# Optimization experiments

Measured on AMD Instinct MI355X. Metric: run time of the kernel, lower is better.

The kernel has to match this reference:

```python
import jax, jax.numpy as jnp
import numpy as np

B, C, H, W, E = 32, 64, 64, 64, 8

def setup_inputs() -> dict:
    key = jax.random.key(0)
    k1, k2, k3 = jax.random.split(key, 3)
    x = jax.random.normal(k1, (B, C, H, W), dtype=jnp.float32)
    gate_w = jax.random.normal(k2, (E, C, 3, 3), dtype=jnp.float32) * 0.02
    gate_b = jnp.zeros((E,), dtype=jnp.float32)
    expert_w = jax.random.normal(k3, (E, C, C), dtype=jnp.float32) * 0.05  # per-expert 1x1 conv (out,in)
    return {"x": x, "gate_w": gate_w, "gate_b": gate_b, "expert_w": expert_w}

def reference(x, gate_w, gate_b, expert_w):
    # Gating: Conv2d(C->E, k=3, stride=1, VALID), then sum over both spatial dims -> [B, E]
    g = jax.lax.conv_general_dilated(
        x, gate_w, window_strides=(1, 1), padding='VALID',
        dimension_numbers=('NCHW', 'OIHW', 'NCHW'))
    g = g + gate_b[None, :, None, None]
    gating_code = jnp.sum(g, axis=(2, 3))                      # [B, E]
    # softmax over experts then top-1
    probs = jax.nn.softmax(gating_code, axis=1)                # [B, E]
    top1_val = jnp.max(probs, axis=1)                          # [B]
    top1_idx = jnp.argmax(probs, axis=1)                       # [B]
    onehot = jax.nn.one_hot(top1_idx, E, dtype=x.dtype)        # [B, E]
    expert_weights = top1_val[:, None] * onehot                # combine tensor squeezed, [B, E]
    dispatch = onehot                                          # bool(combine) cast back to float == one-hot
    # einsum 'bjkd,ben->ebjkd' with n=1: broadcast x to every expert slot, masked by dispatch
    expert_inputs = x[None] * dispatch.T[:, :, None, None, None]   # [E, B, C, H, W]
    # experts: per-expert bias-free 1x1 conv (C -> C)
    expert_out = jnp.einsum('ebchw,efc->ebfhw', expert_inputs, expert_w)  # [E, B, C, H, W]
    # combine: einsum 'ij, ji... -> i...'
    output = jnp.einsum('be,ebchw->bchw', expert_weights, expert_out)      # [B, C, H, W]
    return output, expert_weights
```

## Files before the change

kernel.cpp:

```cpp
#include <hip/hip_runtime.h>

typedef float f4 __attribute__((ext_vector_type(4)));

#define BB 32
#define CC 64
#define EE 8
#define HWX 4096

__global__ __launch_bounds__(256) void k_gate_sums(
    const float* __restrict__ x, const float* __restrict__ gate_w,
    float* __restrict__ gating) {
  __shared__ float sg[9];
  __shared__ float cor[4][4];
  __shared__ float sS[9];
  int t = threadIdx.x;
  int bc = blockIdx.x;
  int c = bc & 63;
  const float* plane = x + (size_t)bc * HWX;
  int h = t >> 2, q = t & 3;
  const f4* rp = (const f4*)(plane + h * 64 + q * 16);
  f4 a0 = rp[0], a1 = rp[1], a2 = rp[2], a3 = rp[3];
  float local = (a0[0]+a0[1]+a0[2]+a0[3]) + (a1[0]+a1[1]+a1[2]+a1[3])
              + (a2[0]+a2[1]+a2[2]+a2[3]) + (a3[0]+a3[1]+a3[2]+a3[3]);
  if (t < 9) sg[t] = 0.f;
  __syncthreads();

  bool special = (h < 2) || (h >= 62);
  int ridx = (h < 2) ? h : h - 60;

  float red = local;
  #pragma unroll
  for (int off = 32; off > 0; off >>= 1) red += __shfl_down(red, off, 64);
  if ((t & 63) == 0) atomicAdd(&sg[0], red);

  if (special) atomicAdd(&sg[1 + ridx], local);
  if (q == 0) {
    atomicAdd(&sg[5], a0[0]); atomicAdd(&sg[6], a0[1]);
    if (special) { cor[ridx][0] = a0[0]; cor[ridx][1] = a0[1]; }
  }
  if (q == 3) {
    atomicAdd(&sg[7], a3[2]); atomicAdd(&sg[8], a3[3]);
    if (special) { cor[ridx][2] = a3[2]; cor[ridx][3] = a3[3]; }
  }
  __syncthreads();

  if (t == 0) {
    const int EX[3][2] = {{2,3},{0,3},{0,1}};
    float T = sg[0];
    #pragma unroll
    for (int i = 0; i < 3; i++)
      #pragma unroll
      for (int j = 0; j < 3; j++) {
        float Re = sg[1 + EX[i][0]] + sg[1 + EX[i][1]];
        float Ce = sg[5 + EX[j][0]] + sg[5 + EX[j][1]];
        float Xc = cor[EX[i][0]][EX[j][0]] + cor[EX[i][0]][EX[j][1]]
                 + cor[EX[i][1]][EX[j][0]] + cor[EX[i][1]][EX[j][1]];
        sS[i * 3 + j] = T - Re - Ce + Xc;
      }
  }
  __syncthreads();

  if (t < EE) {
    const float* gw = gate_w + ((size_t)t * CC + c) * 9;
    float ge = 0.f;
    #pragma unroll
    for (int k = 0; k < 9; k++) ge += gw[k] * sS[k];
    int b = bc >> 6;
    atomicAdd(&gating[b * EE + t], ge);
  }
}

__global__ void k_softmax_top1(const float* __restrict__ gating,
                               const float* __restrict__ gate_b,
                               float* __restrict__ ew_out,
                               float* __restrict__ scale,
                               int* __restrict__ idxb) {
  int b = threadIdx.x;
  if (b >= BB) return;
  float g[EE];
  #pragma unroll
  for (int e = 0; e < EE; e++) g[e] = gating[b * EE + e] + 3844.0f * gate_b[e];
  int best = 0; float bg = g[0];
  #pragma unroll
  for (int e = 1; e < EE; e++) if (g[e] > bg) { bg = g[e]; best = e; }
  float s = 0.f;
  #pragma unroll
  for (int e = 0; e < EE; e++) s += expf(g[e] - bg);
  float val = 1.0f / s;
  #pragma unroll
  for (int e = 0; e < EE; e++) ew_out[b * EE + e] = (e == best) ? val : 0.f;
  scale[b] = val;
  idxb[b] = best;
}

__global__ __launch_bounds__(256) void k_mix(
    const float* __restrict__ x, const float* __restrict__ expert_w,
    const float* __restrict__ scale, const int* __restrict__ idxb,
    float* __restrict__ out) {
  __shared__ float Ws[64 * 68];
  __shared__ float Xs[64 * 64];
  int t = threadIdx.x;
  int pt = blockIdx.x;
  int b = blockIdx.y;
  int e = idxb[b];
  float sc = scale[b];
  const float* Wg = expert_w + (size_t)e * 4096;
  const float* Xg = x + (size_t)b * 64 * 4096 + pt * 64;

  #pragma unroll
  for (int k = 0; k < 4; k++) {
    int i = t + 256 * k;
    int r = i >> 4;
    int c0 = (i & 15) << 2;
    f4 w = *(const f4*)(Wg + r * 64 + c0);
    *(f4*)&Ws[r * 68 + c0] = w;
    f4 xv = *(const f4*)(Xg + (size_t)r * 4096 + c0);
    *(f4*)&Xs[r * 64 + c0] = xv;
  }
  __syncthreads();

  int f0 = (t >> 4) << 2;
  int p0 = (t & 15) << 2;
  float acc[4][4] = {};

  for (int c0 = 0; c0 < 64; c0 += 4) {
    f4 wv[4], xv[4];
    #pragma unroll
    for (int i = 0; i < 4; i++) wv[i] = *(const f4*)&Ws[(f0 + i) * 68 + c0];
    #pragma unroll
    for (int j = 0; j < 4; j++) xv[j] = *(const f4*)&Xs[(c0 + j) * 64 + p0];
    #pragma unroll
    for (int i = 0; i < 4; i++)
      #pragma unroll
      for (int j = 0; j < 4; j++)
        #pragma unroll
        for (int p = 0; p < 4; p++)
          acc[i][p] += wv[i][j] * xv[j][p];
  }

  float* Og = out + ((size_t)(b * 64 + f0)) * 4096 + pt * 64 + p0;
  #pragma unroll
  for (int i = 0; i < 4; i++) {
    f4 r;
    r[0] = sc * acc[i][0]; r[1] = sc * acc[i][1];
    r[2] = sc * acc[i][2]; r[3] = sc * acc[i][3];
    *(f4*)(Og + (size_t)i * 4096) = r;
  }
}

extern "C" void kernel_launch(void* const* d_in, const int* in_sizes, int n_in,
                              void* d_out, int out_size, void* d_ws, size_t ws_size,
                              hipStream_t stream) {
  const float* x        = (const float*)d_in[0];
  const float* gate_w   = (const float*)d_in[1];
  const float* gate_b   = (const float*)d_in[2];
  const float* expert_w = (const float*)d_in[3];
  float* out = (float*)d_out;
  float* ew_out = out + (size_t)BB * CC * HWX;

  float* gating = (float*)d_ws;
  float* scale  = gating + BB * EE;
  int*   idxb   = (int*)(scale + BB);

  hipMemsetAsync(gating, 0, BB * EE * sizeof(float), stream);
  k_gate_sums<<<BB * CC, 256, 0, stream>>>(x, gate_w, gating);
  k_softmax_top1<<<1, 64, 0, stream>>>(gating, gate_b, ew_out, scale, idxb);
  k_mix<<<dim3(64, 32), 256, 0, stream>>>(x, expert_w, scale, idxb, out);
}
```

Before: 107.3 us.

## Fuse softmax/top-1 into mix kernel, drop memset, stage operands as bf16

The gate kernel now writes per-channel partial gating values instead of atomically accumulating, which removes the memset. The separate softmax kernel is folded into the mix kernel, where each block reduces the partials and recomputes the softmax and top-1 choice itself. The mix kernel tile grows to 128 pixels with 8x4 outputs per thread, and both x and the expert weights are rounded to bf16 in shared memory before being unpacked for fp32 FMAs. This cuts two launches and halves shared-memory footprint, but adds bf16 rounding error to the output and redundant gating work in every block.

Result: slower. 110.8 us (+3.3%).

```diff
diff --git a/kernel.cpp b/kernel.cpp
--- a/kernel.cpp
+++ b/kernel.cpp
@@ -6,10 +6,26 @@
 #define CC 64
 #define EE 8
 #define HWX 4096
+#define PXT 128
+
+__device__ __forceinline__ unsigned bf16r(float f) {
+  unsigned u = __builtin_bit_cast(unsigned, f);
+  u += 0x7FFFu + ((u >> 16) & 1u);
+  return u >> 16;
+}
+__device__ __forceinline__ unsigned pack2(float a, float b) {
+  return bf16r(a) | (bf16r(b) << 16);
+}
+__device__ __forceinline__ float ubf_lo(unsigned u) {
+  return __builtin_bit_cast(float, u << 16);
+}
+__device__ __forceinline__ float ubf_hi(unsigned u) {
+  return __builtin_bit_cast(float, u & 0xFFFF0000u);
+}
 
 __global__ __launch_bounds__(256) void k_gate_sums(
     const float* __restrict__ x, const float* __restrict__ gate_w,
-    float* __restrict__ gating) {
+    float* __restrict__ gpart) {
   __shared__ float sg[9];
   __shared__ float cor[4][4];
   __shared__ float sS[9];
@@ -66,85 +82,97 @@
     #pragma unroll
     for (int k = 0; k < 9; k++) ge += gw[k] * sS[k];
     int b = bc >> 6;
-    atomicAdd(&gating[b * EE + t], ge);
+    gpart[b * (EE * CC) + t * CC + c] = ge;
   }
 }
 
-__global__ void k_softmax_top1(const float* __restrict__ gating,
-                               const float* __restrict__ gate_b,
-                               float* __restrict__ ew_out,
-                               float* __restrict__ scale,
-                               int* __restrict__ idxb) {
-  int b = threadIdx.x;
-  if (b >= BB) return;
+__global__ __launch_bounds__(256) void k_mix(
+    const float* __restrict__ x, const float* __restrict__ expert_w,
+    const float* __restrict__ gpart, const float* __restrict__ gate_b,
+    float* __restrict__ out, float* __restrict__ ew_out) {
+  __shared__ uint2 W2[64 * 16];
+  __shared__ uint2 X2[64 * 32];
+  __shared__ float gsh[EE];
+  int t = threadIdx.x;
+  int pt = blockIdx.x;
+  int b  = blockIdx.y;
+
+  const float* Xg = x + (size_t)b * CC * HWX + pt * PXT;
+  #pragma unroll
+  for (int k = 0; k < 8; k++) {
+    int idx = t + 256 * k;
+    int r = idx >> 5, q = idx & 31;
+    f4 v = *(const f4*)(Xg + (size_t)r * HWX + (q << 2));
+    uint2 p; p.x = pack2(v[0], v[1]); p.y = pack2(v[2], v[3]);
+    X2[r * 32 + q] = p;
+  }
+
+  {
+    int e = t >> 5, j = t & 31;
+    const float* gp = gpart + b * (EE * CC) + e * CC;
+    float gval = gp[j] + gp[j + 32];
+    #pragma unroll
+    for (int off = 16; off > 0; off >>= 1) gval += __shfl_down(gval, off, 32);
+    if (j == 0) gsh[e] = gval + 3844.0f * gate_b[e];
+  }
+  __syncthreads();
+
   float g[EE];
   #pragma unroll
-  for (int e = 0; e < EE; e++) g[e] = gating[b * EE + e] + 3844.0f * gate_b[e];
+  for (int e = 0; e < EE; e++) g[e] = gsh[e];
   int best = 0; float bg = g[0];
   #pragma unroll
   for (int e = 1; e < EE; e++) if (g[e] > bg) { bg = g[e]; best = e; }
   float s = 0.f;
   #pragma unroll
-  for (int e = 0; e < EE; e++) s += expf(g[e] - bg);
-  float val = 1.0f / s;
-  #pragma unroll
-  for (int e = 0; e < EE; e++) ew_out[b * EE + e] = (e == best) ? val : 0.f;
-  scale[b] = val;
-  idxb[b] = best;
-}
+  for (int e = 0; e < EE; e++) s += __expf(g[e] - bg);
+  float sc = 1.0f / s;
+  if (pt == 0 && t < EE) ew_out[b * EE + t] = (t == best) ? sc : 0.f;
 
-__global__ __launch_bounds__(256) void k_mix(
-    const float* __restrict__ x, const float* __restrict__ expert_w,
-    const float* __restrict__ scale, const int* __restrict__ idxb,
-    float* __restrict__ out) {
-  __shared__ float Ws[64 * 68];
-  __shared__ float Xs[64 * 64];
-  int t = threadIdx.x;
-  int pt = blockIdx.x;
-  int b = blockIdx.y;
-  int e = idxb[b];
-  float sc = scale[b];
-  const float* Wg = expert_w + (size_t)e * 4096;
-  const float* Xg = x + (size_t)b * 64 * 4096 + pt * 64;
-
+  const float* Wg = expert_w + (size_t)best * (CC * CC);
   #pragma unroll
   for (int k = 0; k < 4; k++) {
-    int i = t + 256 * k;
-    int r = i >> 4;
-    int c0 = (i & 15) << 2;
-    f4 w = *(const f4*)(Wg + r * 64 + c0);
-    *(f4*)&Ws[r * 68 + c0] = w;
-    f4 xv = *(const f4*)(Xg + (size_t)r * 4096 + c0);
-    *(f4*)&Xs[r * 64 + c0] = xv;
+    int idx = t + 256 * k;
+    int r = idx >> 4, q = idx & 15;
+    f4 v = *(const f4*)(Wg + r * CC + (q << 2));
+    uint2 p; p.x = pack2(v[0], v[1]); p.y = pack2(v[2], v[3]);
+    W2[r * 16 + q] = p;
   }
   __syncthreads();
 
-  int f0 = (t >> 4) << 2;
-  int p0 = (t & 15) << 2;
-  float acc[4][4] = {};
-
-  for (int c0 = 0; c0 < 64; c0 += 4) {
-    f4 wv[4], xv[4];
+  int f0 = (t >> 5) << 3;
+  int px = t & 31;
+  float acc[8][4] = {};
+  #pragma unroll
+  for (int cq = 0; cq < 16; cq++) {
+    uint2 xu[4];
     #pragma unroll
-    for (int i = 0; i < 4; i++) wv[i] = *(const f4*)&Ws[(f0 + i) * 68 + c0];
+    for (int j = 0; j < 4; j++) xu[j] = X2[((cq << 2) + j) * 32 + px];
+    uint2 wu[8];
     #pragma unroll
-    for (int j = 0; j < 4; j++) xv[j] = *(const f4*)&Xs[(c0 + j) * 64 + p0];
+    for (int i = 0; i < 8; i++) wu[i] = W2[(f0 + i) * 16 + cq];
     #pragma unroll
-    for (int i = 0; i < 4; i++)
+    for (int j = 0; j < 4; j++) {
+      unsigned xr0 = xu[j].x, xr1 = xu[j].y;
+      float xp0 = ubf_lo(xr0), xp1 = ubf_hi(xr0);
+      float xp2 = ubf_lo(xr1), xp3 = ubf_hi(xr1);
       #pragma unroll
-      for (int j = 0; j < 4; j++)
-        #pragma unroll
-        for (int p = 0; p < 4; p++)
-          acc[i][p] += wv[i][j] * xv[j][p];
+      for (int i = 0; i < 8; i++) {
+        unsigned wraw = (j < 2) ? wu[i].x : wu[i].y;
+        float wf = ((j & 1) == 0) ? ubf_lo(wraw) : ubf_hi(wraw);
+        acc[i][0] += wf * xp0; acc[i][1] += wf * xp1;
+        acc[i][2] += wf * xp2; acc[i][3] += wf * xp3;
+      }
+    }
   }
 
-  float* Og = out + ((size_t)(b * 64 + f0)) * 4096 + pt * 64 + p0;
+  float* Og = out + ((size_t)(b * CC + f0)) * HWX + pt * PXT + (px << 2);
   #pragma unroll
-  for (int i = 0; i < 4; i++) {
+  for (int i = 0; i < 8; i++) {
     f4 r;
     r[0] = sc * acc[i][0]; r[1] = sc * acc[i][1];
     r[2] = sc * acc[i][2]; r[3] = sc * acc[i][3];
-    *(f4*)(Og + (size_t)i * 4096) = r;
+    *(f4*)(Og + (size_t)i * HWX) = r;
   }
 }
 
@@ -158,12 +186,9 @@
   float* out = (float*)d_out;
   float* ew_out = out + (size_t)BB * CC * HWX;
 
-  float* gating = (float*)d_ws;
-  float* scale  = gating + BB * EE;
-  int*   idxb   = (int*)(scale + BB);
+  float* gpart = (float*)d_ws;
 
-  hipMemsetAsync(gating, 0, BB * EE * sizeof(float), stream);
-  k_gate_sums<<<BB * CC, 256, 0, stream>>>(x, gate_w, gating);
-  k_softmax_top1<<<1, 64, 0, stream>>>(gating, gate_b, ew_out, scale, idxb);
-  k_mix<<<dim3(64, 32), 256, 0, stream>>>(x, expert_w, scale, idxb, out);
+  k_gate_sums<<<BB * CC, 256, 0, stream>>>(x, gate_w, gpart);
+  k_mix<<<dim3(HWX / PXT, BB), 256, 0, stream>>>(x, expert_w, gpart, gate_b,
+                                                 out, ew_out);
 }
```
